# Kernel tuning notes

Measured on AMD Instinct MI355X. Metric: run time of the kernel, lower is better.

## Reference

```python
import jax, jax.numpy as jnp
import numpy as np

B, S, H, E, K, D = 1, 4096, 1024, 8, 2, 2048

def setup_inputs() -> dict:
    key = jax.random.key(0)
    k1, k2, k3, k4, k5 = jax.random.split(key, 5)
    x = jax.random.normal(k1, (B, S, H), dtype=jnp.float32)
    attention_mask = jnp.ones((B, S), dtype=jnp.int32)
    expert_weights = jax.random.uniform(k2, (B, S, K), dtype=jnp.float32)
    # distinct top-K expert indices per token (torch code requires at most one match per token)
    r = jax.random.uniform(k3, (B, S, E))
    chosen_expert_indices = jnp.argsort(r, axis=-1)[..., :K].astype(jnp.int64)
    down_proj = jax.random.normal(k4, (E, H, D), dtype=jnp.float32)
    up_proj = jax.random.normal(k5, (E, D, H), dtype=jnp.float32)
    return {"x": x, "attention_mask": attention_mask, "expert_weights": expert_weights,
            "chosen_expert_indices": chosen_expert_indices, "down_proj": down_proj, "up_proj": up_proj}

def reference(x, attention_mask, expert_weights, chosen_expert_indices, down_proj, up_proj):
    b, s, h = x.shape
    e = down_proj.shape[0]
    xt = x.reshape(-1, h)                                   # [N,H]
    n = xt.shape[0]
    mask = attention_mask.reshape(n, 1).astype(x.dtype)     # [N,1]
    idx = chosen_expert_indices.reshape(n, -1)              # [N,K]
    w = expert_weights.reshape(n, -1)                       # [N,K]
    onehot = jax.nn.one_hot(idx, e, dtype=x.dtype)          # [N,K,E]
    # per-token routing weight for each expert (0 if not chosen), masked
    we = jnp.einsum('nk,nke->ne', w, onehot) * mask         # [N,E]
    hid = jax.nn.relu(jnp.einsum('nh,ehd->end', xt, down_proj))  # [E,N,D]
    y = jnp.einsum('end,edh->enh', hid, up_proj)            # [E,N,H]
    mlp = jnp.einsum('ne,enh->nh', we, y)                   # [N,H]
    out = xt + mlp                                          # residual (B==1 as in source)
    return out.reshape(b, s, h)
```

## Files before the change

kernel.cpp:

```cpp
#include <hip/hip_runtime.h>
#include <stdint.h>

#define NTOK 4096
#define HDIM 1024
#define DDIM 2048
#define NEXP 8
#define NASS 8192
#define MAXT 72

typedef __attribute__((ext_vector_type(8))) short bf16x8;
typedef __attribute__((ext_vector_type(4))) float f32x4;

typedef __attribute__((address_space(1))) const unsigned int gu32;
typedef __attribute__((address_space(3))) unsigned int lu32;

__device__ __forceinline__ void async16(void* lds, const void* g) {
  __builtin_amdgcn_global_load_lds((gu32*)(uintptr_t)g, (lu32*)(uintptr_t)lds, 16, 0, 0);
}

__device__ __forceinline__ unsigned short f2bf(float f) {
  unsigned int u = __float_as_uint(f);
  return (unsigned short)((u + 0x7fffu + ((u >> 16) & 1u)) >> 16);
}
__device__ __forceinline__ float bf2f(unsigned short u) {
  return __uint_as_float(((unsigned int)u) << 16);
}

__global__ __launch_bounds__(256) void k_cvt_x(const float* __restrict__ x,
                                               unsigned short* __restrict__ x16) {
  int i = blockIdx.x * 256 + threadIdx.x;
  float4 v = reinterpret_cast<const float4*>(x)[i];
  ushort4 o;
  o.x = f2bf(v.x); o.y = f2bf(v.y); o.z = f2bf(v.z); o.w = f2bf(v.w);
  reinterpret_cast<ushort4*>(x16)[i] = o;
}

__global__ __launch_bounds__(256) void k_transpose(const float* __restrict__ in,
                                                   unsigned short* __restrict__ out,
                                                   int R, int C) {
  __shared__ float t[32][33];
  const size_t mbase = (size_t)blockIdx.z * R * C;
  int tid = threadIdx.x;
  int r = tid >> 3, c4 = (tid & 7) * 4;
  int gr = blockIdx.y * 32 + r;
  int gc = blockIdx.x * 32 + c4;
  float4 v = *reinterpret_cast<const float4*>(in + mbase + (size_t)gr * C + gc);
  t[r][c4 + 0] = v.x; t[r][c4 + 1] = v.y; t[r][c4 + 2] = v.z; t[r][c4 + 3] = v.w;
  __syncthreads();
  int orow = blockIdx.x * 32 + r;
  int oc4  = blockIdx.y * 32 + c4;
  ushort4 o;
  o.x = f2bf(t[c4 + 0][r]); o.y = f2bf(t[c4 + 1][r]);
  o.z = f2bf(t[c4 + 2][r]); o.w = f2bf(t[c4 + 3][r]);
  *reinterpret_cast<ushort4*>(out + mbase + (size_t)orow * R + oc4) = o;
}

__global__ __launch_bounds__(1024) void k_route(
    const int* __restrict__ idx, const float* __restrict__ ew,
    const int* __restrict__ amask,
    int* __restrict__ counts_g, int* __restrict__ offs_g,
    int* __restrict__ toks, float* __restrict__ wl, int* __restrict__ slotmap,
    int* __restrict__ tiles_g, int* __restrict__ ntiles_g) {
  __shared__ int cnt[NEXP], cur[NEXP], flag;
  const int t = threadIdx.x;
  if (t < NEXP) cnt[t] = 0;
  if (t == 0) flag = 0;
  __syncthreads();
  int lf = 0;
#pragma unroll
  for (int j = 0; j < 4; ++j) {
    int i = t + j * 1024;
    if (idx[2 * i + 1] != 0) lf = 1;
  }
  if (lf) atomicOr(&flag, 1);
  __syncthreads();
  const int is32 = flag;
  int e[8];
#pragma unroll
  for (int j = 0; j < 8; ++j) {
    int i = t + j * 1024;
    int ei = is32 ? idx[i] : idx[2 * i];
    e[j] = ei;
    atomicAdd(&cnt[ei], 1);
  }
  __syncthreads();
  if (t == 0) {
    int off = 0, nt_ = 0;
    for (int k = 0; k < NEXP; ++k) {
      cur[k] = off; offs_g[k] = off; counts_g[k] = cnt[k]; off += cnt[k];
      int m = (cnt[k] + 127) >> 7;
      for (int j = 0; j < m; ++j) tiles_g[nt_++] = (k << 16) | j;
    }
    *ntiles_g = nt_;
  }
  __syncthreads();
#pragma unroll
  for (int j = 0; j < 8; ++j) {
    int i = t + j * 1024;
    int n = i >> 1;
    int slot = atomicAdd(&cur[e[j]], 1);
    toks[slot] = n;
    wl[slot] = ew[i] * (amask[n] ? 1.0f : 0.0f);
    slotmap[i] = slot;
  }
}

__global__ __launch_bounds__(256, 2) void k_gemm_down(
    const unsigned short* __restrict__ x16, const unsigned short* __restrict__ bT,
    const int* __restrict__ counts, const int* __restrict__ offs,
    const int* __restrict__ toks, unsigned short* __restrict__ hid,
    const int* __restrict__ tiles, const int* __restrict__ ntiles) {
  const int ti = blockIdx.y;
  if (ti >= *ntiles) return;
  const int pk = tiles[ti];
  const int e = pk >> 16;
  const int mt = pk & 0xffff;
  const int cnt = counts[e];
  const int nt = blockIdx.x;
  const int base = offs[e];
  __shared__ alignas(16) char lds[65536];
  const int tid = threadIdx.x;
  const int lane = tid & 63;
  const int wave = tid >> 6;
  const int wrow = (tid >> 7) * 64;
  const int wcol = ((tid >> 6) & 1) * 64;

  const char* gA[4]; const char* gB[4]; int sOff[4];
  {
    const int swcol = ((lane & 7) << 4) ^ ((lane >> 3) << 4);
#pragma unroll
    for (int it = 0; it < 4; ++it) {
      int row = wave * 32 + it * 8 + (lane >> 3);
      int sl = mt * 128 + row; if (sl >= cnt) sl = cnt - 1;
      gA[it] = (const char*)(x16 + (size_t)toks[base + sl] * HDIM) + swcol;
      gB[it] = (const char*)(bT + (size_t)e * DDIM * HDIM + (size_t)(nt * 128 + row) * HDIM) + swcol;
      sOff[it] = wave * 4096 + it * 1024 + lane * 16;
    }
  }
  const int swz = (lane & 7) << 4;
  const int lo = (lane >> 4) << 4;
  int rowA[4], rowB[4];
#pragma unroll
  for (int m = 0; m < 4; ++m) {
    rowA[m] = (wrow + m * 16 + (lane & 15)) * 128;
    rowB[m] = (wcol + m * 16 + (lane & 15)) * 128;
  }

#pragma unroll
  for (int it = 0; it < 4; ++it) {
    async16(lds + sOff[it], gA[it]);
    async16(lds + 32768 + sOff[it], gB[it]);
  }
  asm volatile("s_waitcnt vmcnt(0)" ::: "memory");
  __builtin_amdgcn_s_barrier();

  f32x4 acc[4][4] = {};
  for (int j = 0; j < 16; ++j) {
    char* curA = lds + ((j & 1) << 14);
    char* curB = lds + 32768 + ((j & 1) << 14);
    char* nxtA = lds + ((~j & 1) << 14);
    char* nxtB = lds + 32768 + ((~j & 1) << 14);
    bf16x8 fa[4], fb[4];
    {
      const int cx = lo ^ swz;
#pragma unroll
      for (int m = 0; m < 4; ++m) fa[m] = *reinterpret_cast<const bf16x8*>(curA + rowA[m] + cx);
#pragma unroll
      for (int n = 0; n < 4; ++n) fb[n] = *reinterpret_cast<const bf16x8*>(curB + rowB[n] + cx);
    }
    if (j < 15) {
      const int ko = (j + 1) << 7;
#pragma unroll
      for (int it = 0; it < 4; ++it) {
        async16(nxtA + sOff[it], gA[it] + ko);
        async16(nxtB + sOff[it], gB[it] + ko);
      }
    }
    __builtin_amdgcn_s_barrier();
    asm volatile("s_waitcnt lgkmcnt(0)" ::: "memory");
    __builtin_amdgcn_sched_barrier(0);
    __builtin_amdgcn_s_setprio(1);
#pragma unroll
    for (int m = 0; m < 4; ++m)
#pragma unroll
      for (int n = 0; n < 4; ++n)
        acc[m][n] = __builtin_amdgcn_mfma_f32_16x16x32_bf16(fa[m], fb[n], acc[m][n], 0, 0, 0);
    __builtin_amdgcn_s_setprio(0);
    __builtin_amdgcn_s_barrier();
    {
      const int cx = (64 | lo) ^ swz;
#pragma unroll
      for (int m = 0; m < 4; ++m) fa[m] = *reinterpret_cast<const bf16x8*>(curA + rowA[m] + cx);
#pragma unroll
      for (int n = 0; n < 4; ++n) fb[n] = *reinterpret_cast<const bf16x8*>(curB + rowB[n] + cx);
    }
    __builtin_amdgcn_s_barrier();
    asm volatile("s_waitcnt lgkmcnt(0)" ::: "memory");
    __builtin_amdgcn_sched_barrier(0);
    __builtin_amdgcn_s_setprio(1);
#pragma unroll
    for (int m = 0; m < 4; ++m)
#pragma unroll
      for (int n = 0; n < 4; ++n)
        acc[m][n] = __builtin_amdgcn_mfma_f32_16x16x32_bf16(fa[m], fb[n], acc[m][n], 0, 0, 0);
    __builtin_amdgcn_s_setprio(0);
    asm volatile("s_waitcnt vmcnt(0)" ::: "memory");
    __builtin_amdgcn_s_barrier();
  }

#pragma unroll
  for (int m = 0; m < 4; ++m) {
    int r0 = mt * 128 + wrow + m * 16 + ((lane >> 4) * 4);
#pragma unroll
    for (int j = 0; j < 4; ++j) {
      int r = r0 + j;
      if (r < cnt) {
        unsigned short* dst = hid + (size_t)(base + r) * DDIM + nt * 128 + wcol + (lane & 15);
#pragma unroll
        for (int n = 0; n < 4; ++n) {
          float v = acc[m][n][j];
          dst[n * 16] = f2bf(v > 0.f ? v : 0.f);
        }
      }
    }
  }
}

__global__ __launch_bounds__(256, 2) void k_gemm_up(
    const unsigned short* __restrict__ hid, const unsigned short* __restrict__ bT,
    const int* __restrict__ counts, const int* __restrict__ offs,
    unsigned short* __restrict__ yw,
    const int* __restrict__ tiles, const int* __restrict__ ntiles) {
  const int ti = blockIdx.y;
  if (ti >= *ntiles) return;
  const int pk = tiles[ti];
  const int e = pk >> 16;
  const int mt = pk & 0xffff;
  const int cnt = counts[e];
  const int ksp = blockIdx.x >> 3;
  const int nt = blockIdx.x & 7;
  const int base = offs[e];
  __shared__ alignas(16) char lds[65536];
  const int tid = threadIdx.x;
  const int lane = tid & 63;
  const int wave = tid >> 6;
  const int wrow = (tid >> 7) * 64;
  const int wcol = ((tid >> 6) & 1) * 64;

  const char* gA[4]; const char* gB[4]; int sOff[4];
  {
    const int swcol = ((lane & 7) << 4) ^ ((lane >> 3) << 4);
#pragma unroll
    for (int it = 0; it < 4; ++it) {
      int row = wave * 32 + it * 8 + (lane >> 3);
      int sl = mt * 128 + row; if (sl >= cnt) sl = cnt - 1;
      gA[it] = (const char*)(hid + (size_t)(base + sl) * DDIM + ksp * 1024) + swcol;
      gB[it] = (const char*)(bT + (size_t)e * HDIM * DDIM + (size_t)(nt * 128 + row) * DDIM + ksp * 1024) + swcol;
      sOff[it] = wave * 4096 + it * 1024 + lane * 16;
    }
  }
  const int swz = (lane & 7) << 4;
  const int lo = (lane >> 4) << 4;
  int rowA[4], rowB[4];
#pragma unroll
  for (int m = 0; m < 4; ++m) {
    rowA[m] = (wrow + m * 16 + (lane & 15)) * 128;
    rowB[m] = (wcol + m * 16 + (lane & 15)) * 128;
  }

#pragma unroll
  for (int it = 0; it < 4; ++it) {
    async16(lds + sOff[it], gA[it]);
    async16(lds + 32768 + sOff[it], gB[it]);
  }
  asm volatile("s_waitcnt vmcnt(0)" ::: "memory");
  __builtin_amdgcn_s_barrier();

  f32x4 acc[4][4] = {};
  for (int j = 0; j < 16; ++j) {
    char* curA = lds + ((j & 1) << 14);
    char* curB = lds + 32768 + ((j & 1) << 14);
    char* nxtA = lds + ((~j & 1) << 14);
    char* nxtB = lds + 32768 + ((~j & 1) << 14);
    bf16x8 fa[4], fb[4];
    {
      const int cx = lo ^ swz;
#pragma unroll
      for (int m = 0; m < 4; ++m) fa[m] = *reinterpret_cast<const bf16x8*>(curA + rowA[m] + cx);
#pragma unroll
      for (int n = 0; n < 4; ++n) fb[n] = *reinterpret_cast<const bf16x8*>(curB + rowB[n] + cx);
    }
    if (j < 15) {
      const int ko = (j + 1) << 7;
#pragma unroll
      for (int it = 0; it < 4; ++it) {
        async16(nxtA + sOff[it], gA[it] + ko);
        async16(nxtB + sOff[it], gB[it] + ko);
      }
    }
    __builtin_amdgcn_s_barrier();
    asm volatile("s_waitcnt lgkmcnt(0)" ::: "memory");
    __builtin_amdgcn_sched_barrier(0);
    __builtin_amdgcn_s_setprio(1);
#pragma unroll
    for (int m = 0; m < 4; ++m)
#pragma unroll
      for (int n = 0; n < 4; ++n)
        acc[m][n] = __builtin_amdgcn_mfma_f32_16x16x32_bf16(fa[m], fb[n], acc[m][n], 0, 0, 0);
    __builtin_amdgcn_s_setprio(0);
    __builtin_amdgcn_s_barrier();
    {
      const int cx = (64 | lo) ^ swz;
#pragma unroll
      for (int m = 0; m < 4; ++m) fa[m] = *reinterpret_cast<const bf16x8*>(curA + rowA[m] + cx);
#pragma unroll
      for (int n = 0; n < 4; ++n) fb[n] = *reinterpret_cast<const bf16x8*>(curB + rowB[n] + cx);
    }
    __builtin_amdgcn_s_barrier();
    asm volatile("s_waitcnt lgkmcnt(0)" ::: "memory");
    __builtin_amdgcn_sched_barrier(0);
    __builtin_amdgcn_s_setprio(1);
#pragma unroll
    for (int m = 0; m < 4; ++m)
#pragma unroll
      for (int n = 0; n < 4; ++n)
        acc[m][n] = __builtin_amdgcn_mfma_f32_16x16x32_bf16(fa[m], fb[n], acc[m][n], 0, 0, 0);
    __builtin_amdgcn_s_setprio(0);
    asm volatile("s_waitcnt vmcnt(0)" ::: "memory");
    __builtin_amdgcn_s_barrier();
  }

#pragma unroll
  for (int m = 0; m < 4; ++m) {
    int r0 = mt * 128 + wrow + m * 16 + ((lane >> 4) * 4);
#pragma unroll
    for (int j = 0; j < 4; ++j) {
      int r = r0 + j;
      if (r < cnt) {
        unsigned short* dst = yw + ((size_t)ksp * NASS + base + r) * HDIM
                              + nt * 128 + wcol + (lane & 15);
#pragma unroll
        for (int n = 0; n < 4; ++n) dst[n * 16] = f2bf(acc[m][n][j]);
      }
    }
  }
}

__global__ __launch_bounds__(256) void k_combine(
    const float* __restrict__ x, const unsigned short* __restrict__ yw,
    const int* __restrict__ slotmap, const float* __restrict__ wl,
    float* __restrict__ out) {
  const int n = blockIdx.x;
  const int t = threadIdx.x;
  const int s0 = slotmap[2 * n], s1 = slotmap[2 * n + 1];
  const float w0 = wl[s0], w1 = wl[s1];
  float4 xv = reinterpret_cast<const float4*>(x + (size_t)n * HDIM)[t];
  ushort4 a0 = reinterpret_cast<const ushort4*>(yw + (size_t)s0 * HDIM)[t];
  ushort4 a1 = reinterpret_cast<const ushort4*>(yw + ((size_t)NASS + s0) * HDIM)[t];
  ushort4 b0 = reinterpret_cast<const ushort4*>(yw + (size_t)s1 * HDIM)[t];
  ushort4 b1 = reinterpret_cast<const ushort4*>(yw + ((size_t)NASS + s1) * HDIM)[t];
  float4 r;
  r.x = xv.x + w0 * (bf2f(a0.x) + bf2f(a1.x)) + w1 * (bf2f(b0.x) + bf2f(b1.x));
  r.y = xv.y + w0 * (bf2f(a0.y) + bf2f(a1.y)) + w1 * (bf2f(b0.y) + bf2f(b1.y));
  r.z = xv.z + w0 * (bf2f(a0.z) + bf2f(a1.z)) + w1 * (bf2f(b0.z) + bf2f(b1.z));
  r.w = xv.w + w0 * (bf2f(a0.w) + bf2f(a1.w)) + w1 * (bf2f(b0.w) + bf2f(b1.w));
  reinterpret_cast<float4*>(out + (size_t)n * HDIM)[t] = r;
}

extern "C" void kernel_launch(void* const* d_in, const int* in_sizes, int n_in,
                              void* d_out, int out_size, void* d_ws, size_t ws_size,
                              hipStream_t stream) {
  const float* x    = (const float*)d_in[0];
  const int* amask  = (const int*)d_in[1];
  const float* ew   = (const float*)d_in[2];
  const int* cidx   = (const int*)d_in[3];
  const float* dn   = (const float*)d_in[4];
  const float* up   = (const float*)d_in[5];
  float* out        = (float*)d_out;
  char* ws          = (char*)d_ws;

  const size_t X16_OFF = 0;
  const size_t DNT_OFF = X16_OFF + (size_t)NTOK * HDIM * 2;
  const size_t UPT_OFF = DNT_OFF + (size_t)NEXP * HDIM * DDIM * 2;
  const size_t HID_OFF = UPT_OFF + (size_t)NEXP * HDIM * DDIM * 2;
  const size_t MET_OFF = HID_OFF + (size_t)NASS * DDIM * 2;

  unsigned short* x16 = (unsigned short*)(ws + X16_OFF);
  unsigned short* dnT = (unsigned short*)(ws + DNT_OFF);
  unsigned short* upT = (unsigned short*)(ws + UPT_OFF);
  unsigned short* hid = (unsigned short*)(ws + HID_OFF);
  unsigned short* yw  = (unsigned short*)(ws + DNT_OFF);
  int* counts  = (int*)(ws + MET_OFF);
  int* offs    = counts + 8;
  int* toks    = counts + 32;
  float* wl    = (float*)(toks + NASS);
  int* slotmap = (int*)(wl + NASS);
  int* tiles   = slotmap + NASS;
  int* ntiles  = tiles + 128;

  k_cvt_x<<<NTOK * HDIM / 1024, 256, 0, stream>>>(x, x16);
  k_transpose<<<dim3(DDIM / 32, HDIM / 32, NEXP), 256, 0, stream>>>(dn, dnT, HDIM, DDIM);
  k_transpose<<<dim3(HDIM / 32, DDIM / 32, NEXP), 256, 0, stream>>>(up, upT, DDIM, HDIM);
  k_route<<<1, 1024, 0, stream>>>(cidx, ew, amask, counts, offs, toks, wl, slotmap,
                                  tiles, ntiles);
  k_gemm_down<<<dim3(16, MAXT), 256, 0, stream>>>(x16, dnT, counts, offs, toks, hid,
                                                  tiles, ntiles);
  k_gemm_up<<<dim3(16, MAXT), 256, 0, stream>>>(hid, upT, counts, offs, yw,
                                                tiles, ntiles);
  k_combine<<<NTOK, 256, 0, stream>>>(x, yw, slotmap, wl, out);
}
```

Baseline: 177.4 us.

## Use 8-wave blocks in expert GEMMs and drop split-K in up projection

Both grouped GEMM kernels now launch 512 threads (8 waves) per 128x128 tile, with each wave computing a 64x32 sub-tile, which halves per-wave accumulators and fragment loads so more waves can hide latency. The up-projection no longer splits K in two: each block loops over the full 2048 depth and writes one bf16 partial, so the combine kernel reads half as much yw data. In exchange the up GEMM launches half as many blocks, each with a longer serial K loop, which lowers parallelism on the GPU. Launch bounds of (512,4) also cap registers per thread.

```diff
diff --git a/kernel.cpp b/kernel.cpp
--- a/kernel.cpp
+++ b/kernel.cpp
@@ -13,6 +13,8 @@
 
 typedef __attribute__((address_space(1))) const unsigned int gu32;
 typedef __attribute__((address_space(3))) unsigned int lu32;
+
+#define BARRIER() asm volatile("s_barrier" ::: "memory")
 
 __device__ __forceinline__ void async16(void* lds, const void* g) {
   __builtin_amdgcn_global_load_lds((gu32*)(uintptr_t)g, (lu32*)(uintptr_t)lds, 16, 0, 0);
@@ -105,7 +107,7 @@
   }
 }
 
-__global__ __launch_bounds__(256, 2) void k_gemm_down(
+__global__ __launch_bounds__(512, 4) void k_gemm_down(
     const unsigned short* __restrict__ x16, const unsigned short* __restrict__ bT,
     const int* __restrict__ counts, const int* __restrict__ offs,
     const int* __restrict__ toks, unsigned short* __restrict__ hid,
@@ -121,103 +123,101 @@
   __shared__ alignas(16) char lds[65536];
   const int tid = threadIdx.x;
   const int lane = tid & 63;
-  const int wave = tid >> 6;
-  const int wrow = (tid >> 7) * 64;
-  const int wcol = ((tid >> 6) & 1) * 64;
-
-  const char* gA[4]; const char* gB[4]; int sOff[4];
+  const int wr = ((tid >> 8) & 1) * 64;
+  const int wc = ((tid >> 6) & 3) * 32;
+
+  const char* gA[2]; const char* gB[2]; int sOff[2];
   {
-    const int swcol = ((lane & 7) << 4) ^ ((lane >> 3) << 4);
-#pragma unroll
-    for (int it = 0; it < 4; ++it) {
-      int row = wave * 32 + it * 8 + (lane >> 3);
+    const int swcol = ((tid & 7) << 4) ^ (((tid >> 3) & 7) << 4);
+#pragma unroll
+    for (int it = 0; it < 2; ++it) {
+      int row = it * 64 + (tid >> 3);
       int sl = mt * 128 + row; if (sl >= cnt) sl = cnt - 1;
       gA[it] = (const char*)(x16 + (size_t)toks[base + sl] * HDIM) + swcol;
       gB[it] = (const char*)(bT + (size_t)e * DDIM * HDIM + (size_t)(nt * 128 + row) * HDIM) + swcol;
-      sOff[it] = wave * 4096 + it * 1024 + lane * 16;
+      sOff[it] = it * 8192 + tid * 16;
     }
   }
   const int swz = (lane & 7) << 4;
   const int lo = (lane >> 4) << 4;
-  int rowA[4], rowB[4];
-#pragma unroll
-  for (int m = 0; m < 4; ++m) {
-    rowA[m] = (wrow + m * 16 + (lane & 15)) * 128;
-    rowB[m] = (wcol + m * 16 + (lane & 15)) * 128;
-  }
-
-#pragma unroll
-  for (int it = 0; it < 4; ++it) {
+  int rowA[4], rowB[2];
+#pragma unroll
+  for (int m = 0; m < 4; ++m) rowA[m] = (wr + m * 16 + (lane & 15)) * 128;
+#pragma unroll
+  for (int n = 0; n < 2; ++n) rowB[n] = (wc + n * 16 + (lane & 15)) * 128;
+
+#pragma unroll
+  for (int it = 0; it < 2; ++it) {
     async16(lds + sOff[it], gA[it]);
     async16(lds + 32768 + sOff[it], gB[it]);
   }
   asm volatile("s_waitcnt vmcnt(0)" ::: "memory");
-  __builtin_amdgcn_s_barrier();
-
-  f32x4 acc[4][4] = {};
+  BARRIER();
+
+  f32x4 acc[4][2] = {};
   for (int j = 0; j < 16; ++j) {
     char* curA = lds + ((j & 1) << 14);
     char* curB = lds + 32768 + ((j & 1) << 14);
     char* nxtA = lds + ((~j & 1) << 14);
     char* nxtB = lds + 32768 + ((~j & 1) << 14);
-    bf16x8 fa[4], fb[4];
+    bf16x8 fa[4], fb[2];
     {
       const int cx = lo ^ swz;
 #pragma unroll
       for (int m = 0; m < 4; ++m) fa[m] = *reinterpret_cast<const bf16x8*>(curA + rowA[m] + cx);
 #pragma unroll
-      for (int n = 0; n < 4; ++n) fb[n] = *reinterpret_cast<const bf16x8*>(curB + rowB[n] + cx);
+      for (int n = 0; n < 2; ++n) fb[n] = *reinterpret_cast<const bf16x8*>(curB + rowB[n] + cx);
     }
     if (j < 15) {
       const int ko = (j + 1) << 7;
 #pragma unroll
-      for (int it = 0; it < 4; ++it) {
+      for (int it = 0; it < 2; ++it) {
         async16(nxtA + sOff[it], gA[it] + ko);
         async16(nxtB + sOff[it], gB[it] + ko);
       }
     }
-    __builtin_amdgcn_s_barrier();
+    BARRIER();
     asm volatile("s_waitcnt lgkmcnt(0)" ::: "memory");
     __builtin_amdgcn_sched_barrier(0);
     __builtin_amdgcn_s_setprio(1);
 #pragma unroll
     for (int m = 0; m < 4; ++m)
 #pragma unroll
-      for (int n = 0; n < 4; ++n)
+      for (int n = 0; n < 2; ++n)
         acc[m][n] = __builtin_amdgcn_mfma_f32_16x16x32_bf16(fa[m], fb[n], acc[m][n], 0, 0, 0);
     __builtin_amdgcn_s_setprio(0);
-    __builtin_amdgcn_s_barrier();
+    BARRIER();
     {
       const int cx = (64 | lo) ^ swz;
 #pragma unroll
       for (int m = 0; m < 4; ++m) fa[m] = *reinterpret_cast<const bf16x8*>(curA + rowA[m] + cx);
 #pragma unroll
-      for (int n = 0; n < 4; ++n) fb[n] = *reinterpret_cast<const bf16x8*>(curB + rowB[n] + cx);
-    }
-    __builtin_amdgcn_s_barrier();
+      for (int n = 0; n < 2; ++n) fb[n] = *reinterpret_cast<const bf16x8*>(curB + rowB[n] + cx);
+    }
+    BARRIER();
     asm volatile("s_waitcnt lgkmcnt(0)" ::: "memory");
     __builtin_amdgcn_sched_barrier(0);
     __builtin_amdgcn_s_setprio(1);
 #pragma unroll
     for (int m = 0; m < 4; ++m)
 #pragma unroll
-      for (int n = 0; n < 4; ++n)
+      for (int n = 0; n < 2; ++n)
         acc[m][n] = __builtin_amdgcn_mfma_f32_16x16x32_bf16(fa[m], fb[n], acc[m][n], 0, 0, 0);
     __builtin_amdgcn_s_setprio(0);
     asm volatile("s_waitcnt vmcnt(0)" ::: "memory");
-    __builtin_amdgcn_s_barrier();
+    BARRIER();
   }
 
 #pragma unroll
   for (int m = 0; m < 4; ++m) {
-    int r0 = mt * 128 + wrow + m * 16 + ((lane >> 4) * 4);
+    int r0 = mt * 128 + wr + m * 16 + ((lane >> 4) * 4);
 #pragma unroll
     for (int j = 0; j < 4; ++j) {
       int r = r0 + j;
       if (r < cnt) {
-        unsigned short* dst = hid + (size_t)(base + r) * DDIM + nt * 128 + wcol + (lane & 15);
-#pragma unroll
-        for (int n = 0; n < 4; ++n) {
+        unsigned short* dst = hid + (size_t)(base + r) * DDIM + nt * 128 + wc + (lane & 15);
+#pragma unroll
+        for (int n = 0; n < 2; ++n) {
           float v = acc[m][n][j];
           dst[n * 16] = f2bf(v > 0.f ? v : 0.f);
         }
@@ -226,7 +226,7 @@
   }
 }
 
-__global__ __launch_bounds__(256, 2) void k_gemm_up(
+__global__ __launch_bounds__(512, 4) void k_gemm_up(
     const unsigned short* __restrict__ hid, const unsigned short* __restrict__ bT,
     const int* __restrict__ counts, const int* __restrict__ offs,
     unsigned short* __restrict__ yw,
@@ -237,110 +237,106 @@
   const int e = pk >> 16;
   const int mt = pk & 0xffff;
   const int cnt = counts[e];
-  const int ksp = blockIdx.x >> 3;
-  const int nt = blockIdx.x & 7;
+  const int nt = blockIdx.x;
   const int base = offs[e];
   __shared__ alignas(16) char lds[65536];
   const int tid = threadIdx.x;
   const int lane = tid & 63;
-  const int wave = tid >> 6;
-  const int wrow = (tid >> 7) * 64;
-  const int wcol = ((tid >> 6) & 1) * 64;
-
-  const char* gA[4]; const char* gB[4]; int sOff[4];
+  const int wr = ((tid >> 8) & 1) * 64;
+  const int wc = ((tid >> 6) & 3) * 32;
+
+  const char* gA[2]; const char* gB[2]; int sOff[2];
   {
-    const int swcol = ((lane & 7) << 4) ^ ((lane >> 3) << 4);
-#pragma unroll
-    for (int it = 0; it < 4; ++it) {
-      int row = wave * 32 + it * 8 + (lane >> 3);
+    const int swcol = ((tid & 7) << 4) ^ (((tid >> 3) & 7) << 4);
+#pragma unroll
+    for (int it = 0; it < 2; ++it) {
+      int row = it * 64 + (tid >> 3);
       int sl = mt * 128 + row; if (sl >= cnt) sl = cnt - 1;
-      gA[it] = (const char*)(hid + (size_t)(base + sl) * DDIM + ksp * 1024) + swcol;
-      gB[it] = (const char*)(bT + (size_t)e * HDIM * DDIM + (size_t)(nt * 128 + row) * DDIM + ksp * 1024) + swcol;
-      sOff[it] = wave * 4096 + it * 1024 + lane * 16;
+      gA[it] = (const char*)(hid + (size_t)(base + sl) * DDIM) + swcol;
+      gB[it] = (const char*)(bT + (size_t)e * HDIM * DDIM + (size_t)(nt * 128 + row) * DDIM) + swcol;
+      sOff[it] = it * 8192 + tid * 16;
     }
   }
   const int swz = (lane & 7) << 4;
   const int lo = (lane >> 4) << 4;
-  int rowA[4], rowB[4];
-#pragma unroll
-  for (int m = 0; m < 4; ++m) {
-    rowA[m] = (wrow + m * 16 + (lane & 15)) * 128;
-    rowB[m] = (wcol + m * 16 + (lane & 15)) * 128;
-  }
-
-#pragma unroll
-  for (int it = 0; it < 4; ++it) {
+  int rowA[4], rowB[2];
+#pragma unroll
+  for (int m = 0; m < 4; ++m) rowA[m] = (wr + m * 16 + (lane & 15)) * 128;
+#pragma unroll
+  for (int n = 0; n < 2; ++n) rowB[n] = (wc + n * 16 + (lane & 15)) * 128;
+
+#pragma unroll
+  for (int it = 0; it < 2; ++it) {
     async16(lds + sOff[it], gA[it]);
     async16(lds + 32768 + sOff[it], gB[it]);
   }
   asm volatile("s_waitcnt vmcnt(0)" ::: "memory");
-  __builtin_amdgcn_s_barrier();
-
-  f32x4 acc[4][4] = {};
-  for (int j = 0; j < 16; ++j) {
+  BARRIER();
+
+  f32x4 acc[4][2] = {};
+  for (int j = 0; j < 32; ++j) {
     char* curA = lds + ((j & 1) << 14);
     char* curB = lds + 32768 + ((j & 1) << 14);
     char* nxtA = lds + ((~j & 1) << 14);
     char* nxtB = lds + 32768 + ((~j & 1) << 14);
-    bf16x8 fa[4], fb[4];
+    bf16x8 fa[4], fb[2];
     {
       const int cx = lo ^ swz;
 #pragma unroll
       for (int m = 0; m < 4; ++m) fa[m] = *reinterpret_cast<const bf16x8*>(curA + rowA[m] + cx);
 #pragma unroll
-      for (int n = 0; n < 4; ++n) fb[n] = *reinterpret_cast<const bf16x8*>(curB + rowB[n] + cx);
-    }
-    if (j < 15) {
+      for (int n = 0; n < 2; ++n) fb[n] = *reinterpret_cast<const bf16x8*>(curB + rowB[n] + cx);
+    }
+    if (j < 31) {
       const int ko = (j + 1) << 7;
 #pragma unroll
-      for (int it = 0; it < 4; ++it) {
+      for (int it = 0; it < 2; ++it) {
         async16(nxtA + sOff[it], gA[it] + ko);
         async16(nxtB + sOff[it], gB[it] + ko);
       }
     }
-    __builtin_amdgcn_s_barrier();
+    BARRIER();
     asm volatile("s_waitcnt lgkmcnt(0)" ::: "memory");
     __builtin_amdgcn_sched_barrier(0);
     __builtin_amdgcn_s_setprio(1);
 #pragma unroll
     for (int m = 0; m < 4; ++m)
 #pragma unroll
-      for (int n = 0; n < 4; ++n)
+      for (int n = 0; n < 2; ++n)
         acc[m][n] = __builtin_amdgcn_mfma_f32_16x16x32_bf16(fa[m], fb[n], acc[m][n], 0, 0, 0);
     __builtin_amdgcn_s_setprio(0);
-    __builtin_amdgcn_s_barrier();
+    BARRIER();
     {
       const int cx = (64 | lo) ^ swz;
 #pragma unroll
       for (int m = 0; m < 4; ++m) fa[m] = *reinterpret_cast<const bf16x8*>(curA + rowA[m] + cx);
 #pragma unroll
-      for (int n = 0; n < 4; ++n) fb[n] = *reinterpret_cast<const bf16x8*>(curB + rowB[n] + cx);
-    }
-    __builtin_amdgcn_s_barrier();
+      for (int n = 0; n < 2; ++n) fb[n] = *reinterpret_cast<const bf16x8*>(curB + rowB[n] + cx);
+    }
+    BARRIER();
     asm volatile("s_waitcnt lgkmcnt(0)" ::: "memory");
     __builtin_amdgcn_sched_barrier(0);
     __builtin_amdgcn_s_setprio(1);
 #pragma unroll
     for (int m = 0; m < 4; ++m)
 #pragma unroll
-      for (int n = 0; n < 4; ++n)
+      for (int n = 0; n < 2; ++n)
         acc[m][n] = __builtin_amdgcn_mfma_f32_16x16x32_bf16(fa[m], fb[n], acc[m][n], 0, 0, 0);
     __builtin_amdgcn_s_setprio(0);
     asm volatile("s_waitcnt vmcnt(0)" ::: "memory");
-    __builtin_amdgcn_s_barrier();
+    BARRIER();
   }
 
 #pragma unroll
   for (int m = 0; m < 4; ++m) {
-    int r0 = mt * 128 + wrow + m * 16 + ((lane >> 4) * 4);
+    int r0 = mt * 128 + wr + m * 16 + ((lane >> 4) * 4);
 #pragma unroll
     for (int j = 0; j < 4; ++j) {
       int r = r0 + j;
       if (r < cnt) {
-        unsigned short* dst = yw + ((size_t)ksp * NASS + base + r) * HDIM
-                              + nt * 128 + wcol + (lane & 15);
-#pragma unroll
-        for (int n = 0; n < 4; ++n) dst[n * 16] = f2bf(acc[m][n][j]);
+        unsigned short* dst = yw + (size_t)(base + r) * HDIM + nt * 128 + wc + (lane & 15);
+#pragma unroll
+        for (int n = 0; n < 2; ++n) dst[n * 16] = f2bf(acc[m][n][j]);
       }
     }
   }
@@ -356,14 +352,12 @@
   const float w0 = wl[s0], w1 = wl[s1];
   float4 xv = reinterpret_cast<const float4*>(x + (size_t)n * HDIM)[t];
   ushort4 a0 = reinterpret_cast<const ushort4*>(yw + (size_t)s0 * HDIM)[t];
-  ushort4 a1 = reinterpret_cast<const ushort4*>(yw + ((size_t)NASS + s0) * HDIM)[t];
   ushort4 b0 = reinterpret_cast<const ushort4*>(yw + (size_t)s1 * HDIM)[t];
-  ushort4 b1 = reinterpret_cast<const ushort4*>(yw + ((size_t)NASS + s1) * HDIM)[t];
   float4 r;
-  r.x = xv.x + w0 * (bf2f(a0.x) + bf2f(a1.x)) + w1 * (bf2f(b0.x) + bf2f(b1.x));
-  r.y = xv.y + w0 * (bf2f(a0.y) + bf2f(a1.y)) + w1 * (bf2f(b0.y) + bf2f(b1.y));
-  r.z = xv.z + w0 * (bf2f(a0.z) + bf2f(a1.z)) + w1 * (bf2f(b0.z) + bf2f(b1.z));
-  r.w = xv.w + w0 * (bf2f(a0.w) + bf2f(a1.w)) + w1 * (bf2f(b0.w) + bf2f(b1.w));
+  r.x = xv.x + w0 * bf2f(a0.x) + w1 * bf2f(b0.x);
+  r.y = xv.y + w0 * bf2f(a0.y) + w1 * bf2f(b0.y);
+  r.z = xv.z + w0 * bf2f(a0.z) + w1 * bf2f(b0.z);
+  r.w = xv.w + w0 * bf2f(a0.w) + w1 * bf2f(b0.w);
   reinterpret_cast<float4*>(out + (size_t)n * HDIM)[t] = r;
 }
 
@@ -403,9 +397,9 @@
   k_transpose<<<dim3(HDIM / 32, DDIM / 32, NEXP), 256, 0, stream>>>(up, upT, DDIM, HDIM);
   k_route<<<1, 1024, 0, stream>>>(cidx, ew, amask, counts, offs, toks, wl, slotmap,
                                   tiles, ntiles);
-  k_gemm_down<<<dim3(16, MAXT), 256, 0, stream>>>(x16, dnT, counts, offs, toks, hid,
+  k_gemm_down<<<dim3(16, MAXT), 512, 0, stream>>>(x16, dnT, counts, offs, toks, hid,
                                                   tiles, ntiles);
-  k_gemm_up<<<dim3(16, MAXT), 256, 0, stream>>>(hid, upT, counts, offs, yw,
-                                                tiles, ntiles);
+  k_gemm_up<<<dim3(8, MAXT), 512, 0, stream>>>(hid, upT, counts, offs, yw,
+                                               tiles, ntiles);
   k_combine<<<NTOK, 256, 0, stream>>>(x, yw, slotmap, wl, out);
 }
```

Measured after the change: 174.4 us. No clear change (-1.7%).
